# Kernel tuning notes

Hardware: AMD Instinct MI355X
Metric: run time of the kernel (lower is better)

Reference implementation:

```python
import jax, jax.numpy as jnp
import numpy as np

N_USER = 100_000
N_ITEM = 50_000
C = 128
E = 600_000
L = 2          # num_layers
NN = 2         # num_layers_nn (MLP depth inside GINConv)
LN_EPS = 1e-5


def _layernorm(x, g, b):
    # PyG LayerNorm(mode='node'): normalize each node over channels, affine
    m = jnp.mean(x, axis=-1, keepdims=True)
    v = jnp.mean((x - m) ** 2, axis=-1, keepdims=True)
    return (x - m) * jax.lax.rsqrt(v + LN_EPS) * g + b


def _mlp(x, W, b):
    # GINConv inner MLP: [Linear -> ReLU] * NN
    for i in range(NN):
        x = jax.nn.relu(x @ W[i] + b[i])
    return x


def setup_inputs() -> dict:
    key = jax.random.key(0)
    ks = jax.random.split(key, 10)
    s = 1.0 / np.sqrt(C)
    edge_ui = jnp.stack([
        jax.random.randint(ks[0], (E,), 0, N_USER, dtype=jnp.int32),  # src: user
        jax.random.randint(ks[1], (E,), 0, N_ITEM, dtype=jnp.int32),  # dst: item
    ])
    edge_iu = jnp.stack([
        jax.random.randint(ks[2], (E,), 0, N_ITEM, dtype=jnp.int32),  # src: item
        jax.random.randint(ks[3], (E,), 0, N_USER, dtype=jnp.int32),  # dst: user
    ])
    return {
        "x_user": jax.random.normal(ks[4], (N_USER, C), dtype=jnp.float32),
        "x_item": jax.random.normal(ks[5], (N_ITEM, C), dtype=jnp.float32),
        "W_init": jax.random.normal(ks[6], (2, C, C), dtype=jnp.float32) * s,
        "b_init": jnp.zeros((2, C), dtype=jnp.float32),
        "mlp_W": jax.random.normal(ks[7], (L, 2, NN, C, C), dtype=jnp.float32) * s,
        "mlp_b": jnp.zeros((L, 2, NN, C), dtype=jnp.float32),
        "eps": jnp.full((L, 2), 1e-5, dtype=jnp.float32),  # train_eps=True, init eps=1e-5
        "ln_g": jnp.ones((L, 2, C), dtype=jnp.float32),
        "ln_b": jnp.zeros((L, 2, C), dtype=jnp.float32),
        "edge_ui": edge_ui,
        "edge_iu": edge_iu,
    }


def reference(x_user, x_item, W_init, b_init, mlp_W, mlp_b, eps, ln_g, ln_b,
              edge_ui, edge_iu):
    # Initial per-node-type projection (LazyLinear)
    xu = x_user @ W_init[0] + b_init[0]
    xi = x_item @ W_init[1] + b_init[1]
    for l in range(L):
        # GINConv per edge type; HeteroConv(aggr='sum') trivially reduces since
        # each node type is targeted by exactly one edge type here.
        agg_i = jax.ops.segment_sum(xu[edge_ui[0]], edge_ui[1], num_segments=N_ITEM)
        agg_u = jax.ops.segment_sum(xi[edge_iu[0]], edge_iu[1], num_segments=N_USER)
        # edge_type index 0 = (user->item), 1 = (item->user)
        new_i = _mlp((1.0 + eps[l, 0]) * xi + agg_i, mlp_W[l, 0], mlp_b[l, 0])
        new_u = _mlp((1.0 + eps[l, 1]) * xu + agg_u, mlp_W[l, 1], mlp_b[l, 1])
        # node_type index 0 = user, 1 = item
        xu = jax.nn.relu(_layernorm(new_u, ln_g[l, 0], ln_b[l, 0]))
        xi = jax.nn.relu(_layernorm(new_i, ln_g[l, 1], ln_b[l, 1]))
    return (xu, xi)
```

## Files before the change

### kernel.cpp

```cpp
#include <hip/hip_runtime.h>
#include <cstdint>
#include <cstddef>

#define N_USER 100000
#define N_ITEM 50000
#define CDIM   128
#define NEDGE  600000
#define N_SEG  (N_ITEM + N_USER)
#define NB_SCAN ((N_SEG + 255) / 256)

#define FILL_EPB 2048
#define FILL_NCHUNK ((NEDGE + FILL_EPB - 1) / FILL_EPB)
#define SLICE_DIV ((N_SEG + 7) / 8)

typedef __bf16 bf16_t;
typedef bf16_t bfvec8 __attribute__((ext_vector_type(8)));
typedef bf16_t bfvec4 __attribute__((ext_vector_type(4)));
typedef float  f32x4  __attribute__((ext_vector_type(4)));

#define LDW 136

static __device__ inline void stage_w(bf16_t* Wt, const float* __restrict__ W, int tid) {
    const f32x4* W4 = reinterpret_cast<const f32x4*>(W);
    #pragma unroll
    for (int i = 0; i < 16; ++i) {
        int cidx = i * 256 + tid;
        int base = cidx * 4;
        int k  = base >> 7;
        int n0 = base & 127;
        f32x4 v = W4[cidx];
        #pragma unroll
        for (int j = 0; j < 4; ++j) Wt[(n0 + j) * LDW + k] = (bf16_t)v[j];
    }
}

__global__ __launch_bounds__(256) void gemm_init(
    const float* __restrict__ X,
    const float* __restrict__ W,
    const float* __restrict__ B,
    bf16_t* __restrict__ Y, int M)
{
    __shared__ __align__(16) bf16_t Wt[128 * LDW];
    const int tid = threadIdx.x;
    stage_w(Wt, W, tid);
    __syncthreads();

    const int wave = tid >> 6, lane = tid & 63;
    const int quad = lane >> 4, ln16 = lane & 15;

    #pragma unroll
    for (int s = 0; s < 2; ++s) {
        int row0 = blockIdx.x * 128 + s * 64 + wave * 16;
        int arow = row0 + ln16;
        int arow_c = arow < M ? arow : 0;

        bfvec8 a[4];
        const float* xp = X + (size_t)arow_c * CDIM + quad * 8;
        #pragma unroll
        for (int kc = 0; kc < 4; ++kc) {
            f32x4 lo = *reinterpret_cast<const f32x4*>(xp + kc * 32);
            f32x4 hi = *reinterpret_cast<const f32x4*>(xp + kc * 32 + 4);
            #pragma unroll
            for (int j = 0; j < 4; ++j) {
                a[kc][j]     = (bf16_t)lo[j];
                a[kc][j + 4] = (bf16_t)hi[j];
            }
        }

        f32x4 acc[8];
        #pragma unroll
        for (int t = 0; t < 8; ++t) acc[t] = (f32x4){0.f, 0.f, 0.f, 0.f};
        #pragma unroll
        for (int t = 0; t < 8; ++t) {
            const bf16_t* wp = &Wt[(t * 16 + ln16) * LDW + quad * 8];
            #pragma unroll
            for (int kc = 0; kc < 4; ++kc) {
                bfvec8 b = *reinterpret_cast<const bfvec8*>(wp + kc * 32);
                acc[t] = __builtin_amdgcn_mfma_f32_16x16x32_bf16(a[kc], b, acc[t], 0, 0, 0);
            }
        }

        if (row0 < M) {
            #pragma unroll
            for (int t = 0; t < 8; ++t) {
                int col = t * 16 + ln16;
                float bias = B[col];
                #pragma unroll
                for (int r = 0; r < 4; ++r) {
                    int row = row0 + quad * 4 + r;
                    if (row < M) Y[(size_t)row * CDIM + col] = (bf16_t)(acc[t][r] + bias);
                }
            }
        }
    }
}

__global__ __launch_bounds__(256) void zero_i32(int* __restrict__ p, int n)
{
    int i = blockIdx.x * 256 + threadIdx.x;
    if (i < n) p[i] = 0;
}

__global__ __launch_bounds__(256) void hist_rank(
    const int* __restrict__ edge_ui, const int* __restrict__ edge_iu,
    int* __restrict__ deg, int2* __restrict__ rank2)
{
    int i = blockIdx.x * 256 + threadIdx.x;
    if (i >= NEDGE) return;
    int r0 = atomicAdd(&deg[edge_ui[NEDGE + i]], 1);
    int r1 = atomicAdd(&deg[N_ITEM + edge_iu[NEDGE + i]], 1);
    rank2[i] = make_int2(r0, r1);
}

__global__ __launch_bounds__(256) void block_scan(
    int* __restrict__ off, int* __restrict__ bsum, int n)
{
    __shared__ int sh[256];
    int tid = threadIdx.x;
    int i = blockIdx.x * 256 + tid;
    int v = (i < n) ? off[i] : 0;
    sh[tid] = v;
    __syncthreads();
    #pragma unroll
    for (int d = 1; d < 256; d <<= 1) {
        int t = (tid >= d) ? sh[tid - d] : 0;
        __syncthreads();
        sh[tid] += t;
        __syncthreads();
    }
    if (i < n) off[i] = sh[tid] - v;
    if (tid == 255) bsum[blockIdx.x] = sh[255];
}

__global__ __launch_bounds__(1024) void scan_bsums(int* __restrict__ bsum)
{
    __shared__ int sh[1024];
    int tid = threadIdx.x;
    int v = (tid < NB_SCAN) ? bsum[tid] : 0;
    sh[tid] = v;
    __syncthreads();
    #pragma unroll
    for (int d = 1; d < 1024; d <<= 1) {
        int t = (tid >= d) ? sh[tid - d] : 0;
        __syncthreads();
        sh[tid] += t;
        __syncthreads();
    }
    if (tid < NB_SCAN) bsum[tid] = sh[tid] - v;
    if (tid == 1023) bsum[NB_SCAN] = sh[1023];
}

__global__ __launch_bounds__(256) void add_offsets(
    int* __restrict__ off, const int* __restrict__ bsum, int n)
{
    int i = blockIdx.x * 256 + threadIdx.x;
    if (i < n) off[i] += bsum[i >> 8];
    else if (i == n) off[n] = bsum[NB_SCAN];
}

__global__ __launch_bounds__(256) void fill_sliced(
    const int* __restrict__ edge_ui, const int* __restrict__ edge_iu,
    const int* __restrict__ off, const int2* __restrict__ rank2,
    int* __restrict__ srcbuf)
{
    const int r = blockIdx.x & 7;
    const int chunk = blockIdx.x >> 3;
    const int base = chunk * FILL_EPB + threadIdx.x;
    #pragma unroll
    for (int j = 0; j < FILL_EPB / 256; ++j) {
        int i = base + j * 256;
        if (i < NEDGE) {
            int d0 = edge_ui[NEDGE + i];
            int d1 = edge_iu[NEDGE + i] + N_ITEM;
            int2 rk = rank2[i];
            if (d0 / SLICE_DIV == r)
                srcbuf[off[d0] + rk.x] = edge_ui[i];
            if (d1 / SLICE_DIV == r)
                srcbuf[off[d1] + rk.y] = edge_iu[i];
        }
    }
}

__global__ __launch_bounds__(256) void gather_both(
    const bf16_t* __restrict__ xu, const bf16_t* __restrict__ xi,
    const float* __restrict__ eps2,
    const int* __restrict__ off_all, const int* __restrict__ srcbuf,
    bf16_t* __restrict__ ti, bf16_t* __restrict__ tu)
{
    const int gBI = (N_ITEM + 3) / 4;
    int b = blockIdx.x;
    bool isItem = b < gBI;
    int wave = threadIdx.x >> 6;
    int node = (isItem ? b : b - gBI) * 4 + wave;
    int n = isItem ? N_ITEM : N_USER;
    if (node >= n) return;

    const bfvec4* F = reinterpret_cast<const bfvec4*>(isItem ? xu : xi);
    const bfvec4* X = reinterpret_cast<const bfvec4*>(isItem ? xi : xu);
    const int* off = isItem ? off_all : off_all + N_ITEM;
    bfvec4* out = reinterpret_cast<bfvec4*>(isItem ? ti : tu);
    float s = 1.f + (isItem ? eps2[0] : eps2[1]);

    int l32  = threadIdx.x & 31;
    int half = (threadIdx.x >> 5) & 1;
    int start = off[node], end = off[node + 1];

    f32x4 acc = (f32x4){0.f, 0.f, 0.f, 0.f};
    int e = start + half;
    for (; e + 6 < end; e += 8) {
        bfvec4 v0 = F[(size_t)srcbuf[e]     * 32 + l32];
        bfvec4 v1 = F[(size_t)srcbuf[e + 2] * 32 + l32];
        bfvec4 v2 = F[(size_t)srcbuf[e + 4] * 32 + l32];
        bfvec4 v3 = F[(size_t)srcbuf[e + 6] * 32 + l32];
        #pragma unroll
        for (int j = 0; j < 4; ++j)
            acc[j] += ((float)v0[j] + (float)v1[j]) + ((float)v2[j] + (float)v3[j]);
    }
    for (; e + 2 < end; e += 4) {
        bfvec4 v0 = F[(size_t)srcbuf[e]     * 32 + l32];
        bfvec4 v1 = F[(size_t)srcbuf[e + 2] * 32 + l32];
        #pragma unroll
        for (int j = 0; j < 4; ++j) acc[j] += (float)v0[j] + (float)v1[j];
    }
    for (; e < end; e += 2) {
        bfvec4 v = F[(size_t)srcbuf[e] * 32 + l32];
        #pragma unroll
        for (int j = 0; j < 4; ++j) acc[j] += (float)v[j];
    }
    #pragma unroll
    for (int j = 0; j < 4; ++j) acc[j] += __shfl_xor(acc[j], 32, 64);

    if (half == 0) {
        bfvec4 xv = X[(size_t)node * 32 + l32];
        bfvec4 o;
        #pragma unroll
        for (int j = 0; j < 4; ++j) o[j] = (bf16_t)(s * (float)xv[j] + acc[j]);
        out[(size_t)node * 32 + l32] = o;
    }
}

__global__ __launch_bounds__(256) void mlp_ln_both(
    const bf16_t* __restrict__ ti, const bf16_t* __restrict__ tu,
    const float* __restrict__ mlpW,
    const float* __restrict__ mlpb,
    const float* __restrict__ lng,
    const float* __restrict__ lnb,
    bf16_t* __restrict__ xib, bf16_t* __restrict__ xub,
    float* __restrict__ xif, float* __restrict__ xuf,
    int f32out)
{
    __shared__ __align__(16) bf16_t Wt[128 * LDW];
    __shared__ __align__(16) bf16_t At[128 * LDW];

    const int gBI = (N_ITEM + 127) / 128;
    int b = blockIdx.x;
    bool isItem = b < gBI;
    const bf16_t* X = isItem ? ti : tu;
    bf16_t* Yb      = isItem ? xib : xub;
    float*  Yf      = isItem ? xif : xuf;
    int M  = isItem ? N_ITEM : N_USER;
    int bx = isItem ? b : b - gBI;
    const float* W1 = mlpW + (isItem ? 0 : 2) * 16384;
    const float* W2 = W1 + 16384;
    const float* B1 = mlpb + (isItem ? 0 : 2) * 128;
    const float* B2 = B1 + 128;
    const float* G  = lng + (isItem ? 128 : 0);
    const float* Bb = lnb + (isItem ? 128 : 0);

    const int tid = threadIdx.x;
    stage_w(Wt, W1, tid);
    __syncthreads();

    const int wave = tid >> 6, lane = tid & 63;
    const int quad = lane >> 4, ln16 = lane & 15;
    const int rowBase = bx * 128;

    #pragma unroll
    for (int s = 0; s < 2; ++s) {
        int row0l = s * 64 + wave * 16;
        int arow = rowBase + row0l + ln16;
        int arow_c = arow < M ? arow : 0;

        bfvec8 a[4];
        const bf16_t* xp = X + (size_t)arow_c * CDIM + quad * 8;
        #pragma unroll
        for (int kc = 0; kc < 4; ++kc)
            a[kc] = *reinterpret_cast<const bfvec8*>(xp + kc * 32);

        f32x4 acc[8];
        #pragma unroll
        for (int t = 0; t < 8; ++t) acc[t] = (f32x4){0.f, 0.f, 0.f, 0.f};
        #pragma unroll
        for (int t = 0; t < 8; ++t) {
            const bf16_t* wp = &Wt[(t * 16 + ln16) * LDW + quad * 8];
            #pragma unroll
            for (int kc = 0; kc < 4; ++kc) {
                bfvec8 bv = *reinterpret_cast<const bfvec8*>(wp + kc * 32);
                acc[t] = __builtin_amdgcn_mfma_f32_16x16x32_bf16(a[kc], bv, acc[t], 0, 0, 0);
            }
        }

        #pragma unroll
        for (int t = 0; t < 8; ++t) {
            int col = t * 16 + ln16;
            float bias = B1[col];
            #pragma unroll
            for (int r = 0; r < 4; ++r) {
                float v = acc[t][r] + bias;
                v = v > 0.f ? v : 0.f;
                At[(row0l + quad * 4 + r) * LDW + col] = (bf16_t)v;
            }
        }
    }
    __syncthreads();
    stage_w(Wt, W2, tid);
    __syncthreads();

    #pragma unroll
    for (int s = 0; s < 2; ++s) {
        int row0l = s * 64 + wave * 16;
        int ml = row0l + ln16;

        bfvec8 a[4];
        #pragma unroll
        for (int kc = 0; kc < 4; ++kc)
            a[kc] = *reinterpret_cast<const bfvec8*>(&At[ml * LDW + kc * 32 + quad * 8]);

        f32x4 acc[8];
        #pragma unroll
        for (int t = 0; t < 8; ++t) acc[t] = (f32x4){0.f, 0.f, 0.f, 0.f};
        #pragma unroll
        for (int t = 0; t < 8; ++t) {
            const bf16_t* wp = &Wt[(t * 16 + ln16) * LDW + quad * 8];
            #pragma unroll
            for (int kc = 0; kc < 4; ++kc) {
                bfvec8 bv = *reinterpret_cast<const bfvec8*>(wp + kc * 32);
                acc[t] = __builtin_amdgcn_mfma_f32_16x16x32_bf16(a[kc], bv, acc[t], 0, 0, 0);
            }
        }

        float gA[8], bA[8];
        #pragma unroll
        for (int t = 0; t < 8; ++t) {
            int col = t * 16 + ln16;
            float b2 = B2[col];
            #pragma unroll
            for (int r = 0; r < 4; ++r) {
                float v = acc[t][r] + b2;
                acc[t][r] = v > 0.f ? v : 0.f;
            }
            gA[t] = G[col]; bA[t] = Bb[col];
        }

        #pragma unroll
        for (int r = 0; r < 4; ++r) {
            float sm = 0.f;
            #pragma unroll
            for (int t = 0; t < 8; ++t) sm += acc[t][r];
            #pragma unroll
            for (int m = 8; m >= 1; m >>= 1) sm += __shfl_xor(sm, m, 16);
            float mean = sm * (1.f / 128.f);
            float sq = 0.f;
            #pragma unroll
            for (int t = 0; t < 8; ++t) { float d = acc[t][r] - mean; sq += d * d; }
            #pragma unroll
            for (int m = 8; m >= 1; m >>= 1) sq += __shfl_xor(sq, m, 16);
            float rs = rsqrtf(sq * (1.f / 128.f) + 1e-5f);

            int row = rowBase + row0l + quad * 4 + r;
            if (row < M) {
                if (f32out) {
                    #pragma unroll
                    for (int t = 0; t < 8; ++t) {
                        float y = (acc[t][r] - mean) * rs * gA[t] + bA[t];
                        y = y > 0.f ? y : 0.f;
                        Yf[(size_t)row * CDIM + t * 16 + ln16] = y;
                    }
                } else {
                    #pragma unroll
                    for (int t = 0; t < 8; ++t) {
                        float y = (acc[t][r] - mean) * rs * gA[t] + bA[t];
                        y = y > 0.f ? y : 0.f;
                        Yb[(size_t)row * CDIM + t * 16 + ln16] = (bf16_t)y;
                    }
                }
            }
        }
    }
}

extern "C" void kernel_launch(void* const* d_in, const int* in_sizes, int n_in,
                              void* d_out, int out_size, void* d_ws, size_t ws_size,
                              hipStream_t stream)
{
    const float* x_user = (const float*)d_in[0];
    const float* x_item = (const float*)d_in[1];
    const float* W_init = (const float*)d_in[2];
    const float* b_init = (const float*)d_in[3];
    const float* mlp_W  = (const float*)d_in[4];
    const float* mlp_b  = (const float*)d_in[5];
    const float* eps    = (const float*)d_in[6];
    const float* ln_g   = (const float*)d_in[7];
    const float* ln_b   = (const float*)d_in[8];
    const int* edge_ui  = (const int*)d_in[9];
    const int* edge_iu  = (const int*)d_in[10];

    float* xuf = (float*)d_out;
    float* xif = xuf + (size_t)N_USER * CDIM;

    char* w = (char*)d_ws;
    bf16_t* xub = (bf16_t*)w;
    bf16_t* xib = xub + (size_t)N_USER * CDIM;
    bf16_t* tub = xib + (size_t)N_ITEM * CDIM;
    bf16_t* tib = tub + (size_t)N_USER * CDIM;
    int* off_all = (int*)(tib + (size_t)N_ITEM * CDIM);
    int* bsum    = off_all + (N_SEG + 4);
    int* srcbuf  = bsum + (NB_SCAN + 2);

    int2* rank2 = (int2*)tub;

    const int gU = (N_USER + 127) / 128;
    const int gI = (N_ITEM + 127) / 128;
    const int gSeg = (N_SEG + 256) / 256;
    const int gE = (NEDGE + 255) / 256;
    const int gGather = (N_ITEM + 3) / 4 + (N_USER + 3) / 4;

    zero_i32<<<(N_SEG + 255) / 256, 256, 0, stream>>>(off_all, N_SEG);
    hist_rank<<<gE, 256, 0, stream>>>(edge_ui, edge_iu, off_all, rank2);
    block_scan<<<NB_SCAN, 256, 0, stream>>>(off_all, bsum, N_SEG);
    scan_bsums<<<1, 1024, 0, stream>>>(bsum);
    add_offsets<<<gSeg, 256, 0, stream>>>(off_all, bsum, N_SEG);
    fill_sliced<<<FILL_NCHUNK * 8, 256, 0, stream>>>(edge_ui, edge_iu, off_all, rank2, srcbuf);

    gemm_init<<<gU, 256, 0, stream>>>(x_user, W_init,         b_init,       xub, N_USER);
    gemm_init<<<gI, 256, 0, stream>>>(x_item, W_init + 16384, b_init + 128, xib, N_ITEM);

    for (int l = 0; l < 2; ++l) {
        gather_both<<<gGather, 256, 0, stream>>>(
            xub, xib, eps + 2 * l, off_all, srcbuf, tib, tub);
        mlp_ln_both<<<gI + gU, 256, 0, stream>>>(
            tib, tub, mlp_W + (size_t)l * 4 * 16384, mlp_b + l * 4 * 128,
            ln_g + l * 2 * 128, ln_b + l * 2 * 128,
            xib, xub, xif, xuf, (l == 1) ? 1 : 0);
    }
}
```

Before: 577.1 us.

## Pre-transpose weights to bf16 once, swap MFMA operands for row-contiguous vectorized stores

Adds a prep kernel that converts and transposes all weight matrices to bf16 once per call, so each GEMM block copies them into shared memory with plain 16-byte vector copies instead of doing strided float-to-bf16 scatter writes. The MFMA operands are swapped so each lane holds four consecutive output columns of one row. This allows vectorized bias loads and output stores, and makes the LayerNorm reduction only two cross-lane shuffles. Blocks grow to 512 threads and each wave handles one 16-row tile, which adds an extra kernel launch and changes occupancy in exchange.

```diff
diff --git a/kernel.cpp b/kernel.cpp
--- a/kernel.cpp
+++ b/kernel.cpp
@@ -20,77 +20,80 @@
 
 #define LDW 136
 
-static __device__ inline void stage_w(bf16_t* Wt, const float* __restrict__ W, int tid) {
-    const f32x4* W4 = reinterpret_cast<const f32x4*>(W);
-    #pragma unroll
-    for (int i = 0; i < 16; ++i) {
-        int cidx = i * 256 + tid;
-        int base = cidx * 4;
-        int k  = base >> 7;
-        int n0 = base & 127;
-        f32x4 v = W4[cidx];
-        #pragma unroll
-        for (int j = 0; j < 4; ++j) Wt[(n0 + j) * LDW + k] = (bf16_t)v[j];
-    }
-}
-
-__global__ __launch_bounds__(256) void gemm_init(
+__global__ __launch_bounds__(256) void prep_weights(
+    const float* __restrict__ W_init, const float* __restrict__ mlp_W,
+    bf16_t* __restrict__ wtg)
+{
+    int m  = blockIdx.x >> 6;
+    int it = blockIdx.x & 63;
+    const float* src = (m < 2) ? (W_init + (size_t)m * 16384)
+                               : (mlp_W + (size_t)(m - 2) * 16384);
+    int e = it * 256 + threadIdx.x;
+    int n = e >> 7, k = e & 127;
+    wtg[(size_t)m * 16384 + e] = (bf16_t)src[k * 128 + n];
+}
+
+template <int NT>
+static __device__ inline void stage_wbf(bf16_t* Wt, const bf16_t* __restrict__ Wg, int tid) {
+    #pragma unroll
+    for (int c = tid; c < 2048; c += NT) {
+        int n = c >> 4, koff = (c & 15) * 8;
+        *reinterpret_cast<bfvec8*>(&Wt[n * LDW + koff]) =
+            *reinterpret_cast<const bfvec8*>(&Wg[n * 128 + koff]);
+    }
+}
+
+__global__ __launch_bounds__(512) void gemm_init(
     const float* __restrict__ X,
-    const float* __restrict__ W,
+    const bf16_t* __restrict__ Wg,
     const float* __restrict__ B,
     bf16_t* __restrict__ Y, int M)
 {
     __shared__ __align__(16) bf16_t Wt[128 * LDW];
     const int tid = threadIdx.x;
-    stage_w(Wt, W, tid);
+    stage_wbf<512>(Wt, Wg, tid);
     __syncthreads();
 
     const int wave = tid >> 6, lane = tid & 63;
     const int quad = lane >> 4, ln16 = lane & 15;
-
-    #pragma unroll
-    for (int s = 0; s < 2; ++s) {
-        int row0 = blockIdx.x * 128 + s * 64 + wave * 16;
-        int arow = row0 + ln16;
-        int arow_c = arow < M ? arow : 0;
-
-        bfvec8 a[4];
-        const float* xp = X + (size_t)arow_c * CDIM + quad * 8;
+    const int row_l = wave * 16 + ln16;
+    const int rowg = blockIdx.x * 128 + row_l;
+    const int rowc = rowg < M ? rowg : 0;
+
+    bfvec8 xb[4];
+    const float* xp = X + (size_t)rowc * CDIM + quad * 8;
+    #pragma unroll
+    for (int kc = 0; kc < 4; ++kc) {
+        f32x4 lo = *reinterpret_cast<const f32x4*>(xp + kc * 32);
+        f32x4 hi = *reinterpret_cast<const f32x4*>(xp + kc * 32 + 4);
+        #pragma unroll
+        for (int j = 0; j < 4; ++j) {
+            xb[kc][j]     = (bf16_t)lo[j];
+            xb[kc][j + 4] = (bf16_t)hi[j];
+        }
+    }
+
+    f32x4 acc[8];
+    #pragma unroll
+    for (int t = 0; t < 8; ++t) acc[t] = (f32x4){0.f, 0.f, 0.f, 0.f};
+    #pragma unroll
+    for (int t = 0; t < 8; ++t) {
+        const bf16_t* wp = &Wt[(t * 16 + ln16) * LDW + quad * 8];
         #pragma unroll
         for (int kc = 0; kc < 4; ++kc) {
-            f32x4 lo = *reinterpret_cast<const f32x4*>(xp + kc * 32);
-            f32x4 hi = *reinterpret_cast<const f32x4*>(xp + kc * 32 + 4);
+            bfvec8 wv = *reinterpret_cast<const bfvec8*>(wp + kc * 32);
+            acc[t] = __builtin_amdgcn_mfma_f32_16x16x32_bf16(wv, xb[kc], acc[t], 0, 0, 0);
+        }
+    }
+
+    if (rowg < M) {
+        #pragma unroll
+        for (int t = 0; t < 8; ++t) {
+            f32x4 bv = *reinterpret_cast<const f32x4*>(&B[t * 16 + quad * 4]);
+            bfvec4 o;
             #pragma unroll
-            for (int j = 0; j < 4; ++j) {
-                a[kc][j]     = (bf16_t)lo[j];
-                a[kc][j + 4] = (bf16_t)hi[j];
-            }
-        }
-
-        f32x4 acc[8];
-        #pragma unroll
-        for (int t = 0; t < 8; ++t) acc[t] = (f32x4){0.f, 0.f, 0.f, 0.f};
-        #pragma unroll
-        for (int t = 0; t < 8; ++t) {
-            const bf16_t* wp = &Wt[(t * 16 + ln16) * LDW + quad * 8];
-            #pragma unroll
-            for (int kc = 0; kc < 4; ++kc) {
-                bfvec8 b = *reinterpret_cast<const bfvec8*>(wp + kc * 32);
-                acc[t] = __builtin_amdgcn_mfma_f32_16x16x32_bf16(a[kc], b, acc[t], 0, 0, 0);
-            }
-        }
-
-        if (row0 < M) {
-            #pragma unroll
-            for (int t = 0; t < 8; ++t) {
-                int col = t * 16 + ln16;
-                float bias = B[col];
-                #pragma unroll
-                for (int r = 0; r < 4; ++r) {
-                    int row = row0 + quad * 4 + r;
-                    if (row < M) Y[(size_t)row * CDIM + col] = (bf16_t)(acc[t][r] + bias);
-                }
-            }
+            for (int r = 0; r < 4; ++r) o[r] = (bf16_t)(acc[t][r] + bv[r]);
+            *reinterpret_cast<bfvec4*>(&Y[(size_t)rowg * CDIM + t * 16 + quad * 4]) = o;
         }
     }
 }
@@ -239,9 +242,9 @@
     }
 }
 
-__global__ __launch_bounds__(256) void mlp_ln_both(
+__global__ __launch_bounds__(512) void mlp_ln_both(
     const bf16_t* __restrict__ ti, const bf16_t* __restrict__ tu,
-    const float* __restrict__ mlpW,
+    const bf16_t* __restrict__ wg,
     const float* __restrict__ mlpb,
     const float* __restrict__ lng,
     const float* __restrict__ lnb,
@@ -260,130 +263,127 @@
     float*  Yf      = isItem ? xif : xuf;
     int M  = isItem ? N_ITEM : N_USER;
     int bx = isItem ? b : b - gBI;
-    const float* W1 = mlpW + (isItem ? 0 : 2) * 16384;
-    const float* W2 = W1 + 16384;
+    const bf16_t* W1 = wg + (isItem ? 0 : 2) * 16384;
+    const bf16_t* W2 = W1 + 16384;
     const float* B1 = mlpb + (isItem ? 0 : 2) * 128;
     const float* B2 = B1 + 128;
     const float* G  = lng + (isItem ? 128 : 0);
     const float* Bb = lnb + (isItem ? 128 : 0);
 
     const int tid = threadIdx.x;
-    stage_w(Wt, W1, tid);
+    stage_wbf<512>(Wt, W1, tid);
     __syncthreads();
 
     const int wave = tid >> 6, lane = tid & 63;
     const int quad = lane >> 4, ln16 = lane & 15;
-    const int rowBase = bx * 128;
-
-    #pragma unroll
-    for (int s = 0; s < 2; ++s) {
-        int row0l = s * 64 + wave * 16;
-        int arow = rowBase + row0l + ln16;
-        int arow_c = arow < M ? arow : 0;
-
-        bfvec8 a[4];
-        const bf16_t* xp = X + (size_t)arow_c * CDIM + quad * 8;
-        #pragma unroll
-        for (int kc = 0; kc < 4; ++kc)
-            a[kc] = *reinterpret_cast<const bfvec8*>(xp + kc * 32);
-
-        f32x4 acc[8];
-        #pragma unroll
-        for (int t = 0; t < 8; ++t) acc[t] = (f32x4){0.f, 0.f, 0.f, 0.f};
-        #pragma unroll
-        for (int t = 0; t < 8; ++t) {
-            const bf16_t* wp = &Wt[(t * 16 + ln16) * LDW + quad * 8];
+    const int row_l = wave * 16 + ln16;
+    const int rowg = bx * 128 + row_l;
+    const int rowc = rowg < M ? rowg : 0;
+
+    bfvec8 xb[4];
+    const bf16_t* xp = X + (size_t)rowc * CDIM + quad * 8;
+    #pragma unroll
+    for (int kc = 0; kc < 4; ++kc)
+        xb[kc] = *reinterpret_cast<const bfvec8*>(xp + kc * 32);
+
+    f32x4 acc[8];
+    #pragma unroll
+    for (int t = 0; t < 8; ++t) acc[t] = (f32x4){0.f, 0.f, 0.f, 0.f};
+    #pragma unroll
+    for (int t = 0; t < 8; ++t) {
+        const bf16_t* wp = &Wt[(t * 16 + ln16) * LDW + quad * 8];
+        #pragma unroll
+        for (int kc = 0; kc < 4; ++kc) {
+            bfvec8 wv = *reinterpret_cast<const bfvec8*>(wp + kc * 32);
+            acc[t] = __builtin_amdgcn_mfma_f32_16x16x32_bf16(wv, xb[kc], acc[t], 0, 0, 0);
+        }
+    }
+
+    #pragma unroll
+    for (int t = 0; t < 8; ++t) {
+        f32x4 bv = *reinterpret_cast<const f32x4*>(&B1[t * 16 + quad * 4]);
+        bfvec4 o;
+        #pragma unroll
+        for (int r = 0; r < 4; ++r) {
+            float v = acc[t][r] + bv[r];
+            o[r] = (bf16_t)(v > 0.f ? v : 0.f);
+        }
+        *reinterpret_cast<bfvec4*>(&At[row_l * LDW + t * 16 + quad * 4]) = o;
+    }
+    __syncthreads();
+    stage_wbf<512>(Wt, W2, tid);
+    __syncthreads();
+
+    bfvec8 hb[4];
+    #pragma unroll
+    for (int kc = 0; kc < 4; ++kc)
+        hb[kc] = *reinterpret_cast<const bfvec8*>(&At[row_l * LDW + kc * 32 + quad * 8]);
+
+    #pragma unroll
+    for (int t = 0; t < 8; ++t) acc[t] = (f32x4){0.f, 0.f, 0.f, 0.f};
+    #pragma unroll
+    for (int t = 0; t < 8; ++t) {
+        const bf16_t* wp = &Wt[(t * 16 + ln16) * LDW + quad * 8];
+        #pragma unroll
+        for (int kc = 0; kc < 4; ++kc) {
+            bfvec8 wv = *reinterpret_cast<const bfvec8*>(wp + kc * 32);
+            acc[t] = __builtin_amdgcn_mfma_f32_16x16x32_bf16(wv, hb[kc], acc[t], 0, 0, 0);
+        }
+    }
+
+    #pragma unroll
+    for (int t = 0; t < 8; ++t) {
+        f32x4 bv = *reinterpret_cast<const f32x4*>(&B2[t * 16 + quad * 4]);
+        #pragma unroll
+        for (int r = 0; r < 4; ++r) {
+            float v = acc[t][r] + bv[r];
+            acc[t][r] = v > 0.f ? v : 0.f;
+        }
+    }
+
+    float sm = 0.f;
+    #pragma unroll
+    for (int t = 0; t < 8; ++t)
+        #pragma unroll
+        for (int r = 0; r < 4; ++r) sm += acc[t][r];
+    sm += __shfl_xor(sm, 16, 64);
+    sm += __shfl_xor(sm, 32, 64);
+    float mean = sm * (1.f / 128.f);
+    float sq = 0.f;
+    #pragma unroll
+    for (int t = 0; t < 8; ++t)
+        #pragma unroll
+        for (int r = 0; r < 4; ++r) { float d = acc[t][r] - mean; sq += d * d; }
+    sq += __shfl_xor(sq, 16, 64);
+    sq += __shfl_xor(sq, 32, 64);
+    float rs = rsqrtf(sq * (1.f / 128.f) + 1e-5f);
+
+    if (rowg < M) {
+        if (f32out) {
             #pragma unroll
-            for (int kc = 0; kc < 4; ++kc) {
-                bfvec8 bv = *reinterpret_cast<const bfvec8*>(wp + kc * 32);
-                acc[t] = __builtin_amdgcn_mfma_f32_16x16x32_bf16(a[kc], bv, acc[t], 0, 0, 0);
+            for (int t = 0; t < 8; ++t) {
+                f32x4 g4 = *reinterpret_cast<const f32x4*>(&G[t * 16 + quad * 4]);
+                f32x4 b4 = *reinterpret_cast<const f32x4*>(&Bb[t * 16 + quad * 4]);
+                f32x4 y;
+                #pragma unroll
+                for (int r = 0; r < 4; ++r) {
+                    float v = (acc[t][r] - mean) * rs * g4[r] + b4[r];
+                    y[r] = v > 0.f ? v : 0.f;
+                }
+                *reinterpret_cast<f32x4*>(&Yf[(size_t)rowg * CDIM + t * 16 + quad * 4]) = y;
             }
-        }
-
-        #pragma unroll
-        for (int t = 0; t < 8; ++t) {
-            int col = t * 16 + ln16;
-            float bias = B1[col];
+        } else {
             #pragma unroll
-            for (int r = 0; r < 4; ++r) {
-                float v = acc[t][r] + bias;
-                v = v > 0.f ? v : 0.f;
-                At[(row0l + quad * 4 + r) * LDW + col] = (bf16_t)v;
-            }
-        }
-    }
-    __syncthreads();
-    stage_w(Wt, W2, tid);
-    __syncthreads();
-
-    #pragma unroll
-    for (int s = 0; s < 2; ++s) {
-        int row0l = s * 64 + wave * 16;
-        int ml = row0l + ln16;
-
-        bfvec8 a[4];
-        #pragma unroll
-        for (int kc = 0; kc < 4; ++kc)
-            a[kc] = *reinterpret_cast<const bfvec8*>(&At[ml * LDW + kc * 32 + quad * 8]);
-
-        f32x4 acc[8];
-        #pragma unroll
-        for (int t = 0; t < 8; ++t) acc[t] = (f32x4){0.f, 0.f, 0.f, 0.f};
-        #pragma unroll
-        for (int t = 0; t < 8; ++t) {
-            const bf16_t* wp = &Wt[(t * 16 + ln16) * LDW + quad * 8];
-            #pragma unroll
-            for (int kc = 0; kc < 4; ++kc) {
-                bfvec8 bv = *reinterpret_cast<const bfvec8*>(wp + kc * 32);
-                acc[t] = __builtin_amdgcn_mfma_f32_16x16x32_bf16(a[kc], bv, acc[t], 0, 0, 0);
-            }
-        }
-
-        float gA[8], bA[8];
-        #pragma unroll
-        for (int t = 0; t < 8; ++t) {
-            int col = t * 16 + ln16;
-            float b2 = B2[col];
-            #pragma unroll
-            for (int r = 0; r < 4; ++r) {
-                float v = acc[t][r] + b2;
-                acc[t][r] = v > 0.f ? v : 0.f;
-            }
-            gA[t] = G[col]; bA[t] = Bb[col];
-        }
-
-        #pragma unroll
-        for (int r = 0; r < 4; ++r) {
-            float sm = 0.f;
-            #pragma unroll
-            for (int t = 0; t < 8; ++t) sm += acc[t][r];
-            #pragma unroll
-            for (int m = 8; m >= 1; m >>= 1) sm += __shfl_xor(sm, m, 16);
-            float mean = sm * (1.f / 128.f);
-            float sq = 0.f;
-            #pragma unroll
-            for (int t = 0; t < 8; ++t) { float d = acc[t][r] - mean; sq += d * d; }
-            #pragma unroll
-            for (int m = 8; m >= 1; m >>= 1) sq += __shfl_xor(sq, m, 16);
-            float rs = rsqrtf(sq * (1.f / 128.f) + 1e-5f);
-
-            int row = rowBase + row0l + quad * 4 + r;
-            if (row < M) {
-                if (f32out) {
-                    #pragma unroll
-                    for (int t = 0; t < 8; ++t) {
-                        float y = (acc[t][r] - mean) * rs * gA[t] + bA[t];
-                        y = y > 0.f ? y : 0.f;
-                        Yf[(size_t)row * CDIM + t * 16 + ln16] = y;
-                    }
-                } else {
-                    #pragma unroll
-                    for (int t = 0; t < 8; ++t) {
-                        float y = (acc[t][r] - mean) * rs * gA[t] + bA[t];
-                        y = y > 0.f ? y : 0.f;
-                        Yb[(size_t)row * CDIM + t * 16 + ln16] = (bf16_t)y;
-                    }
+            for (int t = 0; t < 8; ++t) {
+                f32x4 g4 = *reinterpret_cast<const f32x4*>(&G[t * 16 + quad * 4]);
+                f32x4 b4 = *reinterpret_cast<const f32x4*>(&Bb[t * 16 + quad * 4]);
+                bfvec4 y;
+                #pragma unroll
+                for (int r = 0; r < 4; ++r) {
+                    float v = (acc[t][r] - mean) * rs * g4[r] + b4[r];
+                    y[r] = (bf16_t)(v > 0.f ? v : 0.f);
                 }
+                *reinterpret_cast<bfvec4*>(&Yb[(size_t)rowg * CDIM + t * 16 + quad * 4]) = y;
             }
         }
     }
@@ -416,6 +416,7 @@
     int* off_all = (int*)(tib + (size_t)N_ITEM * CDIM);
     int* bsum    = off_all + (N_SEG + 4);
     int* srcbuf  = bsum + (NB_SCAN + 2);
+    bf16_t* wtg  = (bf16_t*)(srcbuf + 2 * NEDGE);
 
     int2* rank2 = (int2*)tub;
 
@@ -424,6 +425,8 @@
     const int gSeg = (N_SEG + 256) / 256;
     const int gE = (NEDGE + 255) / 256;
     const int gGather = (N_ITEM + 3) / 4 + (N_USER + 3) / 4;
+
+    prep_weights<<<640, 256, 0, stream>>>(W_init, mlp_W, wtg);
 
     zero_i32<<<(N_SEG + 255) / 256, 256, 0, stream>>>(off_all, N_SEG);
     hist_rank<<<gE, 256, 0, stream>>>(edge_ui, edge_iu, off_all, rank2);
@@ -432,14 +435,14 @@
     add_offsets<<<gSeg, 256, 0, stream>>>(off_all, bsum, N_SEG);
     fill_sliced<<<FILL_NCHUNK * 8, 256, 0, stream>>>(edge_ui, edge_iu, off_all, rank2, srcbuf);
 
-    gemm_init<<<gU, 256, 0, stream>>>(x_user, W_init,         b_init,       xub, N_USER);
-    gemm_init<<<gI, 256, 0, stream>>>(x_item, W_init + 16384, b_init + 128, xib, N_ITEM);
+    gemm_init<<<gU, 512, 0, stream>>>(x_user, wtg,         b_init,       xub, N_USER);
+    gemm_init<<<gI, 512, 0, stream>>>(x_item, wtg + 16384, b_init + 128, xib, N_ITEM);
 
     for (int l = 0; l < 2; ++l) {
         gather_both<<<gGather, 256, 0, stream>>>(
             xub, xib, eps + 2 * l, off_all, srcbuf, tib, tub);
-        mlp_ln_both<<<gI + gU, 256, 0, stream>>>(
-            tib, tub, mlp_W + (size_t)l * 4 * 16384, mlp_b + l * 4 * 128,
+        mlp_ln_both<<<gI + gU, 512, 0, stream>>>(
+            tib, tub, wtg + (size_t)(2 + l * 4) * 16384, mlp_b + l * 4 * 128,
             ln_g + l * 2 * 128, ln_b + l * 2 * 128,
             xib, xub, xif, xuf, (l == 1) ? 1 : 0);
     }
```

Result: faster. 472.1 us (-18.2%).
